# Kernel optimization log

Hardware: AMD Instinct MI355X
Metric: run time of the kernel (lower is better)

## Reference

```python
import jax, jax.numpy as jnp
import numpy as np

N_NODES = 50000
N_EDGES = 600000
D_IN = 128
D_OUT = 128
BN_EPS = 1e-5


def setup_inputs() -> dict:
    key = jax.random.key(0)
    k1, k2, k3, k4 = jax.random.split(key, 4)
    x = jax.random.normal(k1, (N_NODES, D_IN), dtype=jnp.float32)
    edge_index = jax.random.randint(k2, (2, N_EDGES), 0, N_NODES, dtype=jnp.int64)
    W = jax.random.normal(k3, (D_OUT, D_IN), dtype=jnp.float32) * (1.0 / np.sqrt(D_IN))
    b = jax.random.normal(k4, (D_OUT,), dtype=jnp.float32) * 0.01
    gamma = jnp.ones((D_OUT,), dtype=jnp.float32)
    beta = jnp.zeros((D_OUT,), dtype=jnp.float32)
    return {"x": x, "edge_index": edge_index, "W": W, "b": b, "gamma": gamma, "beta": beta}


def reference(x, edge_index, W, b, gamma, beta):
    n = x.shape[0]
    row, col = edge_index[0], edge_index[1]
    # degree of each destination node, clamped to >= 1
    deg = jnp.clip(jnp.bincount(row, length=n).astype(x.dtype), 1.0, None)
    # gather neighbor features and scatter-add by destination (row)
    agg = jax.ops.segment_sum(x[col], row, num_segments=n)  # [N, D_in]
    h = x + agg / deg[:, None]
    # linear: h @ W.T + b
    y = jnp.einsum('nd,od->no', h, W) + b  # [N, D_out]
    # BatchNorm1d (training mode: batch stats, biased variance)
    mean = jnp.mean(y, axis=0)
    var = jnp.mean((y - mean) ** 2, axis=0)
    y = (y - mean) * jax.lax.rsqrt(var + BN_EPS) * gamma + beta
    return jax.nn.relu(y)
```

## Files before the change

kernel.cpp:

```cpp
#include <hip/hip_runtime.h>

#define NN 50000
#define NE 600000
#define D 128
#define BN_EPS 1e-5f
#define NPART 8
#define KSEG 16

typedef __attribute__((ext_vector_type(8))) short bf16x8;
typedef __attribute__((ext_vector_type(4))) float f32x4;
typedef __attribute__((ext_vector_type(8))) unsigned int uintx8;
typedef unsigned int uint;
typedef unsigned short ushort;

__device__ __forceinline__ ushort f2bf(float f) {
    uint u = __float_as_uint(f);
    uint r = (u + 0x7fffu + ((u >> 16) & 1u)) >> 16;
    return (ushort)r;
}
__device__ __forceinline__ float bflo(uint v) { return __uint_as_float(v << 16); }
__device__ __forceinline__ float bfhi(uint v) { return __uint_as_float(v & 0xffff0000u); }

__global__ __launch_bounds__(256) void prep(const float* __restrict__ x,
                                            const float* __restrict__ W,
                                            uint* __restrict__ xb,
                                            ushort* __restrict__ Wb,
                                            int* __restrict__ deg8,
                                            float* __restrict__ colsum,
                                            float* __restrict__ colsq) {
    int i = blockIdx.x * 256 + threadIdx.x;
    if (i < NN * (D / 4)) {
        float4 v = ((const float4*)x)[i];
        uint2 o;
        o.x = (uint)f2bf(v.x) | ((uint)f2bf(v.y) << 16);
        o.y = (uint)f2bf(v.z) | ((uint)f2bf(v.w) << 16);
        ((uint2*)xb)[i] = o;
    }
    if (i < D * D) Wb[i] = f2bf(W[i]);
    if (i < NPART * NN) deg8[i] = 0;
    if (i < D) { colsum[i] = 0.f; colsq[i] = 0.f; }
}

__global__ __launch_bounds__(256) void bucket_fill(const int* __restrict__ row,
                                                   const int* __restrict__ col,
                                                   int* __restrict__ deg8,
                                                   ushort* __restrict__ adj8) {
    int e = blockIdx.x * 256 + threadIdx.x;
    if (e < NE) {
        int p = blockIdx.x & (NPART - 1);
        int r = row[e];
        int c = col[e];
        int slot = atomicAdd(&deg8[p * NN + r], 1);
        if (slot < KSEG)
            adj8[(((size_t)(p * NN + r)) << 4) + slot] = (ushort)c;
    }
}

__global__ __launch_bounds__(256) void gather_h4(const uint* __restrict__ xb,
                                                 const int* __restrict__ deg8,
                                                 const ushort* __restrict__ adj8,
                                                 uint* __restrict__ hb) {
    int gw = (blockIdx.x * blockDim.x + threadIdx.x) >> 6;
    int lane = threadIdx.x & 63;
    if (gw >= NN) return;
    int qw = lane >> 4;
    int ql = lane & 15;

    int pA = qw, pB = qw + 4;
    int dA = deg8[pA * NN + gw];
    int dB = deg8[pB * NN + gw];
    int cA = (dA < KSEG) ? dA : KSEG;
    int cB = (dB < KSEG) ? dB : KSEG;
    uintx8 wA = *(const uintx8*)(adj8 + (((size_t)(pA * NN + gw)) << 4));
    uintx8 wB = *(const uintx8*)(adj8 + (((size_t)(pB * NN + gw)) << 4));

    uint4 xs = ((const uint4*)(xb + (size_t)gw * (D / 2)))[ql];

    float a[8] = {0.f, 0.f, 0.f, 0.f, 0.f, 0.f, 0.f, 0.f};
    #pragma unroll
    for (int j = 0; j < KSEG; j++) {
        if (j < cA) {
            int nb = (j & 1) ? (int)(wA[j >> 1] >> 16) : (int)(wA[j >> 1] & 0xffffu);
            uint4 v = ((const uint4*)(xb + (size_t)nb * (D / 2)))[ql];
            a[0] += bflo(v.x); a[1] += bfhi(v.x);
            a[2] += bflo(v.y); a[3] += bfhi(v.y);
            a[4] += bflo(v.z); a[5] += bfhi(v.z);
            a[6] += bflo(v.w); a[7] += bfhi(v.w);
        }
    }
    #pragma unroll
    for (int j = 0; j < KSEG; j++) {
        if (j < cB) {
            int nb = (j & 1) ? (int)(wB[j >> 1] >> 16) : (int)(wB[j >> 1] & 0xffffu);
            uint4 v = ((const uint4*)(xb + (size_t)nb * (D / 2)))[ql];
            a[0] += bflo(v.x); a[1] += bfhi(v.x);
            a[2] += bflo(v.y); a[3] += bfhi(v.y);
            a[4] += bflo(v.z); a[5] += bfhi(v.z);
            a[6] += bflo(v.w); a[7] += bfhi(v.w);
        }
    }

    int dsum = dA + dB;
    #pragma unroll
    for (int k = 0; k < 8; k++) {
        a[k] += __shfl_xor(a[k], 16);
        a[k] += __shfl_xor(a[k], 32);
    }
    dsum += __shfl_xor(dsum, 16);
    dsum += __shfl_xor(dsum, 32);

    if (qw == 0) {
        float inv = (dsum > 0) ? (1.0f / (float)dsum) : 0.f;
        uint4 o;
        o.x = (uint)f2bf(bflo(xs.x) + a[0] * inv) | ((uint)f2bf(bfhi(xs.x) + a[1] * inv) << 16);
        o.y = (uint)f2bf(bflo(xs.y) + a[2] * inv) | ((uint)f2bf(bfhi(xs.y) + a[3] * inv) << 16);
        o.z = (uint)f2bf(bflo(xs.z) + a[4] * inv) | ((uint)f2bf(bfhi(xs.z) + a[5] * inv) << 16);
        o.w = (uint)f2bf(bflo(xs.w) + a[6] * inv) | ((uint)f2bf(bfhi(xs.w) + a[7] * inv) << 16);
        ((uint4*)(hb + (size_t)gw * (D / 2)))[ql] = o;
    }
}

__global__ __launch_bounds__(256) void gemm_bn2(const ushort* __restrict__ hb,
                                                const ushort* __restrict__ Wb,
                                                const float* __restrict__ bias,
                                                ushort* __restrict__ yb,
                                                float* __restrict__ colsum,
                                                float* __restrict__ colsq) {
    __shared__ float lsum[D], lsq[D];
    int t = threadIdx.x;
    int lane = t & 63;
    int wv = t >> 6;
    if (t < D) { lsum[t] = 0.f; lsq[t] = 0.f; }
    __syncthreads();

    int row0 = blockIdx.x * 64 + wv * 16;
    int kb = lane >> 4;
    int ar = row0 + (lane & 15);
    if (ar >= NN) ar = NN - 1;

    const bf16x8* hrow = (const bf16x8*)(hb + (size_t)ar * D);
    bf16x8 a0 = hrow[0 * 4 + kb];
    bf16x8 a1 = hrow[1 * 4 + kb];
    bf16x8 a2 = hrow[2 * 4 + kb];
    bf16x8 a3 = hrow[3 * 4 + kb];

    int rbase = row0 + (lane >> 4) * 4;

    #pragma unroll
    for (int nt = 0; nt < 8; nt++) {
        int col = nt * 16 + (lane & 15);
        const bf16x8* wr = (const bf16x8*)(Wb + (size_t)col * D);
        bf16x8 b0 = wr[0 * 4 + kb];
        bf16x8 b1 = wr[1 * 4 + kb];
        bf16x8 b2 = wr[2 * 4 + kb];
        bf16x8 b3 = wr[3 * 4 + kb];

        float bv = bias[col];
        f32x4 acc = {bv, bv, bv, bv};
        acc = __builtin_amdgcn_mfma_f32_16x16x32_bf16(a0, b0, acc, 0, 0, 0);
        acc = __builtin_amdgcn_mfma_f32_16x16x32_bf16(a1, b1, acc, 0, 0, 0);
        acc = __builtin_amdgcn_mfma_f32_16x16x32_bf16(a2, b2, acc, 0, 0, 0);
        acc = __builtin_amdgcn_mfma_f32_16x16x32_bf16(a3, b3, acc, 0, 0, 0);

        float s = 0.f, q = 0.f;
        #pragma unroll
        for (int r = 0; r < 4; r++) {
            int rr = rbase + r;
            if (rr < NN) {
                yb[(size_t)rr * D + col] = f2bf(acc[r]);
                s += acc[r];
                q += acc[r] * acc[r];
            }
        }
        s += __shfl_xor(s, 16); s += __shfl_xor(s, 32);
        q += __shfl_xor(q, 16); q += __shfl_xor(q, 32);
        if (lane < 16) {
            atomicAdd(&lsum[nt * 16 + lane], s);
            atomicAdd(&lsq[nt * 16 + lane], q);
        }
    }
    __syncthreads();
    if (t < D) {
        atomicAdd(&colsum[t], lsum[t]);
        atomicAdd(&colsq[t], lsq[t]);
    }
}

__global__ __launch_bounds__(256) void bn_relu(const uint* __restrict__ yb,
                                               float* __restrict__ out,
                                               const float* __restrict__ colsum,
                                               const float* __restrict__ colsq,
                                               const float* __restrict__ gamma,
                                               const float* __restrict__ beta) {
    int i = blockIdx.x * blockDim.x + threadIdx.x;
    if (i >= NN * D / 4) return;
    uint2 yv = ((const uint2*)yb)[i];
    float yf[4] = {bflo(yv.x), bfhi(yv.x), bflo(yv.y), bfhi(yv.y)};
    int c = (i * 4) & 127;
    float4 v;
    float* vp = (float*)&v;
    #pragma unroll
    for (int j = 0; j < 4; j++) {
        float mean = colsum[c + j] * (1.0f / NN);
        float var  = colsq[c + j] * (1.0f / NN) - mean * mean;
        float sc = gamma[c + j] * rsqrtf(var + BN_EPS);
        float sh = beta[c + j] - mean * sc;
        vp[j] = fmaxf(0.f, yf[j] * sc + sh);
    }
    ((float4*)out)[i] = v;
}

extern "C" void kernel_launch(void* const* d_in, const int* in_sizes, int n_in,
                              void* d_out, int out_size, void* d_ws, size_t ws_size,
                              hipStream_t stream) {
    const float* x     = (const float*)d_in[0];
    const int*   edge  = (const int*)d_in[1];
    const float* W     = (const float*)d_in[2];
    const float* bias  = (const float*)d_in[3];
    const float* gamma = (const float*)d_in[4];
    const float* beta  = (const float*)d_in[5];
    float* out = (float*)d_out;

    const int* row = edge;
    const int* col = edge + NE;

    char* w = (char*)d_ws;
    auto alloc = [&](size_t bytes) {
        char* p = w;
        w += (bytes + 255) & ~(size_t)255;
        return p;
    };
    int*    deg8   = (int*)alloc((size_t)NPART * NN * 4);
    ushort* adj8   = (ushort*)alloc((size_t)NPART * NN * KSEG * 2);
    float*  colsum = (float*)alloc(D * 4);
    float*  colsq  = (float*)alloc(D * 4);
    uint*   xb     = (uint*)alloc((size_t)NN * (D / 2) * 4);
    uint*   hb     = (uint*)alloc((size_t)NN * (D / 2) * 4);
    uint*   yb     = (uint*)alloc((size_t)NN * (D / 2) * 4);
    ushort* Wb     = (ushort*)alloc((size_t)D * D * 2);

    prep<<<(NN * (D / 4) + 255) / 256, 256, 0, stream>>>(x, W, xb, Wb, deg8, colsum, colsq);
    bucket_fill<<<(NE + 255) / 256, 256, 0, stream>>>(row, col, deg8, adj8);
    gather_h4<<<(NN * 64 + 255) / 256, 256, 0, stream>>>(xb, deg8, adj8, hb);
    gemm_bn2<<<(NN + 63) / 64, 256, 0, stream>>>((const ushort*)hb, (const ushort*)Wb,
                                                 bias, (ushort*)yb, colsum, colsq);
    bn_relu<<<(NN * D / 4 + 255) / 256, 256, 0, stream>>>(yb, out, colsum, colsq, gamma, beta);
}
```

Before: 115.0 us.

## Apply linear transform before neighbor aggregation and drop the bias

Uses linearity to compute z = x·Wᵀ first, then aggregates z over neighbors, so the gather works on projected rows. The x-to-bf16 pass is folded into the GEMM, which reads fp32 x directly. The bias is dropped because training-mode BatchNorm subtracts the column mean and cancels it. BN statistics now come from a separate grid-stride pass over y, which adds one more read of y in exchange for removing the separate xb conversion buffer and its write/read round trip.

```diff
diff --git a/kernel.cpp b/kernel.cpp
--- a/kernel.cpp
+++ b/kernel.cpp
@@ -21,21 +21,12 @@
 __device__ __forceinline__ float bflo(uint v) { return __uint_as_float(v << 16); }
 __device__ __forceinline__ float bfhi(uint v) { return __uint_as_float(v & 0xffff0000u); }
 
-__global__ __launch_bounds__(256) void prep(const float* __restrict__ x,
-                                            const float* __restrict__ W,
-                                            uint* __restrict__ xb,
-                                            ushort* __restrict__ Wb,
-                                            int* __restrict__ deg8,
-                                            float* __restrict__ colsum,
-                                            float* __restrict__ colsq) {
+__global__ __launch_bounds__(256) void prep0(const float* __restrict__ W,
+                                             ushort* __restrict__ Wb,
+                                             int* __restrict__ deg8,
+                                             float* __restrict__ colsum,
+                                             float* __restrict__ colsq) {
     int i = blockIdx.x * 256 + threadIdx.x;
-    if (i < NN * (D / 4)) {
-        float4 v = ((const float4*)x)[i];
-        uint2 o;
-        o.x = (uint)f2bf(v.x) | ((uint)f2bf(v.y) << 16);
-        o.y = (uint)f2bf(v.z) | ((uint)f2bf(v.w) << 16);
-        ((uint2*)xb)[i] = o;
-    }
     if (i < D * D) Wb[i] = f2bf(W[i]);
     if (i < NPART * NN) deg8[i] = 0;
     if (i < D) { colsum[i] = 0.f; colsq[i] = 0.f; }
@@ -56,10 +47,61 @@
     }
 }
 
-__global__ __launch_bounds__(256) void gather_h4(const uint* __restrict__ xb,
-                                                 const int* __restrict__ deg8,
-                                                 const ushort* __restrict__ adj8,
-                                                 uint* __restrict__ hb) {
+__global__ __launch_bounds__(256) void gemm_z(const float* __restrict__ x,
+                                              const ushort* __restrict__ Wb,
+                                              ushort* __restrict__ zb) {
+    int t = threadIdx.x;
+    int lane = t & 63;
+    int wv = t >> 6;
+    int row0 = blockIdx.x * 64 + wv * 16;
+    int kb = lane >> 4;
+    int ar = row0 + (lane & 15);
+    if (ar >= NN) ar = NN - 1;
+
+    const float* xr = x + (size_t)ar * D;
+    bf16x8 afr[4];
+    #pragma unroll
+    for (int ks = 0; ks < 4; ks++) {
+        int k0 = ks * 32 + kb * 8;
+        float4 u = *(const float4*)(xr + k0);
+        float4 v = *(const float4*)(xr + k0 + 4);
+        bf16x8 f;
+        f[0] = (short)f2bf(u.x); f[1] = (short)f2bf(u.y);
+        f[2] = (short)f2bf(u.z); f[3] = (short)f2bf(u.w);
+        f[4] = (short)f2bf(v.x); f[5] = (short)f2bf(v.y);
+        f[6] = (short)f2bf(v.z); f[7] = (short)f2bf(v.w);
+        afr[ks] = f;
+    }
+
+    int rbase = row0 + (lane >> 4) * 4;
+
+    #pragma unroll
+    for (int nt = 0; nt < 8; nt++) {
+        int cc = nt * 16 + (lane & 15);
+        const bf16x8* wr = (const bf16x8*)(Wb + (size_t)cc * D);
+        bf16x8 b0 = wr[0 * 4 + kb];
+        bf16x8 b1 = wr[1 * 4 + kb];
+        bf16x8 b2 = wr[2 * 4 + kb];
+        bf16x8 b3 = wr[3 * 4 + kb];
+
+        f32x4 acc = {0.f, 0.f, 0.f, 0.f};
+        acc = __builtin_amdgcn_mfma_f32_16x16x32_bf16(afr[0], b0, acc, 0, 0, 0);
+        acc = __builtin_amdgcn_mfma_f32_16x16x32_bf16(afr[1], b1, acc, 0, 0, 0);
+        acc = __builtin_amdgcn_mfma_f32_16x16x32_bf16(afr[2], b2, acc, 0, 0, 0);
+        acc = __builtin_amdgcn_mfma_f32_16x16x32_bf16(afr[3], b3, acc, 0, 0, 0);
+
+        #pragma unroll
+        for (int r = 0; r < 4; r++) {
+            int rr = rbase + r;
+            if (rr < NN) zb[(size_t)rr * D + cc] = f2bf(acc[r]);
+        }
+    }
+}
+
+__global__ __launch_bounds__(256) void gather_z(const uint* __restrict__ zb,
+                                                const int* __restrict__ deg8,
+                                                const ushort* __restrict__ adj8,
+                                                uint* __restrict__ yb) {
     int gw = (blockIdx.x * blockDim.x + threadIdx.x) >> 6;
     int lane = threadIdx.x & 63;
     if (gw >= NN) return;
@@ -74,14 +116,14 @@
     uintx8 wA = *(const uintx8*)(adj8 + (((size_t)(pA * NN + gw)) << 4));
     uintx8 wB = *(const uintx8*)(adj8 + (((size_t)(pB * NN + gw)) << 4));
 
-    uint4 xs = ((const uint4*)(xb + (size_t)gw * (D / 2)))[ql];
+    uint4 xs = ((const uint4*)(zb + (size_t)gw * (D / 2)))[ql];
 
     float a[8] = {0.f, 0.f, 0.f, 0.f, 0.f, 0.f, 0.f, 0.f};
     #pragma unroll
     for (int j = 0; j < KSEG; j++) {
         if (j < cA) {
             int nb = (j & 1) ? (int)(wA[j >> 1] >> 16) : (int)(wA[j >> 1] & 0xffffu);
-            uint4 v = ((const uint4*)(xb + (size_t)nb * (D / 2)))[ql];
+            uint4 v = ((const uint4*)(zb + (size_t)nb * (D / 2)))[ql];
             a[0] += bflo(v.x); a[1] += bfhi(v.x);
             a[2] += bflo(v.y); a[3] += bfhi(v.y);
             a[4] += bflo(v.z); a[5] += bfhi(v.z);
@@ -92,7 +134,7 @@
     for (int j = 0; j < KSEG; j++) {
         if (j < cB) {
             int nb = (j & 1) ? (int)(wB[j >> 1] >> 16) : (int)(wB[j >> 1] & 0xffffu);
-            uint4 v = ((const uint4*)(xb + (size_t)nb * (D / 2)))[ql];
+            uint4 v = ((const uint4*)(zb + (size_t)nb * (D / 2)))[ql];
             a[0] += bflo(v.x); a[1] += bfhi(v.x);
             a[2] += bflo(v.y); a[3] += bfhi(v.y);
             a[4] += bflo(v.z); a[5] += bfhi(v.z);
@@ -116,68 +158,42 @@
         o.y = (uint)f2bf(bflo(xs.y) + a[2] * inv) | ((uint)f2bf(bfhi(xs.y) + a[3] * inv) << 16);
         o.z = (uint)f2bf(bflo(xs.z) + a[4] * inv) | ((uint)f2bf(bfhi(xs.z) + a[5] * inv) << 16);
         o.w = (uint)f2bf(bflo(xs.w) + a[6] * inv) | ((uint)f2bf(bfhi(xs.w) + a[7] * inv) << 16);
-        ((uint4*)(hb + (size_t)gw * (D / 2)))[ql] = o;
-    }
-}
-
-__global__ __launch_bounds__(256) void gemm_bn2(const ushort* __restrict__ hb,
-                                                const ushort* __restrict__ Wb,
-                                                const float* __restrict__ bias,
-                                                ushort* __restrict__ yb,
-                                                float* __restrict__ colsum,
-                                                float* __restrict__ colsq) {
+        ((uint4*)(yb + (size_t)gw * (D / 2)))[ql] = o;
+    }
+}
+
+__global__ __launch_bounds__(256) void stats(const uint* __restrict__ yb,
+                                             float* __restrict__ colsum,
+                                             float* __restrict__ colsq) {
     __shared__ float lsum[D], lsq[D];
     int t = threadIdx.x;
     int lane = t & 63;
-    int wv = t >> 6;
     if (t < D) { lsum[t] = 0.f; lsq[t] = 0.f; }
     __syncthreads();
 
-    int row0 = blockIdx.x * 64 + wv * 16;
-    int kb = lane >> 4;
-    int ar = row0 + (lane & 15);
-    if (ar >= NN) ar = NN - 1;
-
-    const bf16x8* hrow = (const bf16x8*)(hb + (size_t)ar * D);
-    bf16x8 a0 = hrow[0 * 4 + kb];
-    bf16x8 a1 = hrow[1 * 4 + kb];
-    bf16x8 a2 = hrow[2 * 4 + kb];
-    bf16x8 a3 = hrow[3 * 4 + kb];
-
-    int rbase = row0 + (lane >> 4) * 4;
-
-    #pragma unroll
-    for (int nt = 0; nt < 8; nt++) {
-        int col = nt * 16 + (lane & 15);
-        const bf16x8* wr = (const bf16x8*)(Wb + (size_t)col * D);
-        bf16x8 b0 = wr[0 * 4 + kb];
-        bf16x8 b1 = wr[1 * 4 + kb];
-        bf16x8 b2 = wr[2 * 4 + kb];
-        bf16x8 b3 = wr[3 * 4 + kb];
-
-        float bv = bias[col];
-        f32x4 acc = {bv, bv, bv, bv};
-        acc = __builtin_amdgcn_mfma_f32_16x16x32_bf16(a0, b0, acc, 0, 0, 0);
-        acc = __builtin_amdgcn_mfma_f32_16x16x32_bf16(a1, b1, acc, 0, 0, 0);
-        acc = __builtin_amdgcn_mfma_f32_16x16x32_bf16(a2, b2, acc, 0, 0, 0);
-        acc = __builtin_amdgcn_mfma_f32_16x16x32_bf16(a3, b3, acc, 0, 0, 0);
-
-        float s = 0.f, q = 0.f;
-        #pragma unroll
-        for (int r = 0; r < 4; r++) {
-            int rr = rbase + r;
-            if (rr < NN) {
-                yb[(size_t)rr * D + col] = f2bf(acc[r]);
-                s += acc[r];
-                q += acc[r] * acc[r];
-            }
-        }
-        s += __shfl_xor(s, 16); s += __shfl_xor(s, 32);
-        q += __shfl_xor(q, 16); q += __shfl_xor(q, 32);
-        if (lane < 16) {
-            atomicAdd(&lsum[nt * 16 + lane], s);
-            atomicAdd(&lsq[nt * 16 + lane], q);
-        }
+    const int total = NN * D / 4;
+    int gsz = gridDim.x * 256;
+    int i0 = blockIdx.x * 256 + t;
+    int c = (i0 * 4) & 127;
+    float s0 = 0.f, s1 = 0.f, s2 = 0.f, s3 = 0.f;
+    float q0 = 0.f, q1 = 0.f, q2 = 0.f, q3 = 0.f;
+    for (int i = i0; i < total; i += gsz) {
+        uint2 yv = ((const uint2*)yb)[i];
+        float f0 = bflo(yv.x), f1 = bfhi(yv.x), f2 = bflo(yv.y), f3 = bfhi(yv.y);
+        s0 += f0; q0 += f0 * f0;
+        s1 += f1; q1 += f1 * f1;
+        s2 += f2; q2 += f2 * f2;
+        s3 += f3; q3 += f3 * f3;
+    }
+    s0 += __shfl_xor(s0, 32); q0 += __shfl_xor(q0, 32);
+    s1 += __shfl_xor(s1, 32); q1 += __shfl_xor(q1, 32);
+    s2 += __shfl_xor(s2, 32); q2 += __shfl_xor(q2, 32);
+    s3 += __shfl_xor(s3, 32); q3 += __shfl_xor(q3, 32);
+    if (lane < 32) {
+        atomicAdd(&lsum[c],     s0); atomicAdd(&lsq[c],     q0);
+        atomicAdd(&lsum[c + 1], s1); atomicAdd(&lsq[c + 1], q1);
+        atomicAdd(&lsum[c + 2], s2); atomicAdd(&lsq[c + 2], q2);
+        atomicAdd(&lsum[c + 3], s3); atomicAdd(&lsq[c + 3], q3);
     }
     __syncthreads();
     if (t < D) {
@@ -216,7 +232,6 @@
     const float* x     = (const float*)d_in[0];
     const int*   edge  = (const int*)d_in[1];
     const float* W     = (const float*)d_in[2];
-    const float* bias  = (const float*)d_in[3];
     const float* gamma = (const float*)d_in[4];
     const float* beta  = (const float*)d_in[5];
     float* out = (float*)d_out;
@@ -234,15 +249,14 @@
     ushort* adj8   = (ushort*)alloc((size_t)NPART * NN * KSEG * 2);
     float*  colsum = (float*)alloc(D * 4);
     float*  colsq  = (float*)alloc(D * 4);
-    uint*   xb     = (uint*)alloc((size_t)NN * (D / 2) * 4);
-    uint*   hb     = (uint*)alloc((size_t)NN * (D / 2) * 4);
+    uint*   zb     = (uint*)alloc((size_t)NN * (D / 2) * 4);
     uint*   yb     = (uint*)alloc((size_t)NN * (D / 2) * 4);
     ushort* Wb     = (ushort*)alloc((size_t)D * D * 2);
 
-    prep<<<(NN * (D / 4) + 255) / 256, 256, 0, stream>>>(x, W, xb, Wb, deg8, colsum, colsq);
+    prep0<<<(NPART * NN + 255) / 256, 256, 0, stream>>>(W, Wb, deg8, colsum, colsq);
     bucket_fill<<<(NE + 255) / 256, 256, 0, stream>>>(row, col, deg8, adj8);
-    gather_h4<<<(NN * 64 + 255) / 256, 256, 0, stream>>>(xb, deg8, adj8, hb);
-    gemm_bn2<<<(NN + 63) / 64, 256, 0, stream>>>((const ushort*)hb, (const ushort*)Wb,
-                                                 bias, (ushort*)yb, colsum, colsq);
+    gemm_z<<<(NN + 63) / 64, 256, 0, stream>>>(x, (const ushort*)Wb, (ushort*)zb);
+    gather_z<<<(NN * 64 + 255) / 256, 256, 0, stream>>>(zb, deg8, adj8, yb);
+    stats<<<512, 256, 0, stream>>>(yb, colsum, colsq);
     bn_relu<<<(NN * D / 4 + 255) / 256, 256, 0, stream>>>(yb, out, colsum, colsq, gamma, beta);
 }
```

Result: slower. 119.1 us (+3.6%).
